# Kernel optimization log

Hardware: AMD Instinct MI355X
Metric: run time of the kernel (lower is better)

Reference implementation:

```python
import jax, jax.numpy as jnp
import numpy as np
import math
from jax import lax

B, L, C_IN = 32, 1024, 21
D_MODEL, N_HEADS, D_FF = 512, 8, 2048
E_LAYERS, FACTOR, MA_K = 3, 1, 25
N_CLASSES = 10
EPS = 1e-5


def setup_inputs() -> dict:
    key = jax.random.key(0)
    ks = jax.random.split(key, 12)
    s = 0.02
    return {
        "x_enc": jax.random.normal(ks[0], (B, L, C_IN), jnp.float32),
        "x_mark_enc": jnp.ones((B, L), jnp.float32),
        "conv_emb_w": jax.random.normal(ks[1], (D_MODEL, C_IN, 3), jnp.float32) * s,
        "Wq": jax.random.normal(ks[2], (E_LAYERS, D_MODEL, D_MODEL), jnp.float32) * s,
        "bq": jnp.zeros((E_LAYERS, D_MODEL), jnp.float32),
        "Wk": jax.random.normal(ks[3], (E_LAYERS, D_MODEL, D_MODEL), jnp.float32) * s,
        "bk": jnp.zeros((E_LAYERS, D_MODEL), jnp.float32),
        "Wv": jax.random.normal(ks[4], (E_LAYERS, D_MODEL, D_MODEL), jnp.float32) * s,
        "bv": jnp.zeros((E_LAYERS, D_MODEL), jnp.float32),
        "Wo": jax.random.normal(ks[5], (E_LAYERS, D_MODEL, D_MODEL), jnp.float32) * s,
        "bo": jnp.zeros((E_LAYERS, D_MODEL), jnp.float32),
        "Wff1": jax.random.normal(ks[6], (E_LAYERS, D_FF, D_MODEL), jnp.float32) * s,
        "Wff2": jax.random.normal(ks[7], (E_LAYERS, D_MODEL, D_FF), jnp.float32) * s,
        "ln_g": jnp.ones((D_MODEL,), jnp.float32),
        "ln_b": jnp.zeros((D_MODEL,), jnp.float32),
        "Wproj": jax.random.normal(ks[8], (N_CLASSES, D_MODEL * L), jnp.float32) * 0.001,
        "bproj": jnp.zeros((N_CLASSES,), jnp.float32),
    }


def token_embed(x, w):
    # x: [B, L, C] -> Conv1d(C->D, k=3, circular padding, no bias) -> [B, L, D]
    xp = jnp.pad(x.transpose(0, 2, 1), ((0, 0), (0, 0), (1, 1)), mode='wrap')  # [B,C,L+2]
    y = lax.conv_general_dilated(xp, w, (1,), 'VALID', dimension_numbers=('NCH', 'OIH', 'NCH'))
    return y.transpose(0, 2, 1)


def moving_avg(x, k):
    # replicate-pad then avg-pool with stride 1 (kernel k odd -> same length)
    pad = (k - 1) // 2
    xp = jnp.concatenate([jnp.repeat(x[:, :1], pad, 1), x, jnp.repeat(x[:, -1:], pad, 1)], axis=1)
    return lax.reduce_window(xp, 0.0, lax.add, (1, k, 1), (1, 1, 1), 'VALID') / k


def series_decomp(x, k):
    m = moving_avg(x, k)
    return x - m, m


def auto_correlation(q, k, v):
    # q,k,v: [B, L, H, E]; FFT-based period correlation + time-delay aggregation (inference variant)
    B_, L_, H, E = q.shape
    qf = jnp.fft.rfft(q.transpose(0, 2, 3, 1), axis=-1)   # [B,H,E,Lf]
    kf = jnp.fft.rfft(k.transpose(0, 2, 3, 1), axis=-1)
    corr = jnp.fft.irfft(qf * jnp.conj(kf), n=L_, axis=-1)  # [B,H,E,L]
    values = v.transpose(0, 2, 3, 1)                        # [B,H,E,L]
    mean_value = corr.mean(axis=(1, 2))                     # [B,L]
    top_k = int(FACTOR * math.log(L_))
    weights, delay = lax.top_k(mean_value, top_k)           # [B,k]
    tmp_corr = jax.nn.softmax(weights, axis=-1)
    tmp_values = jnp.concatenate([values, values], axis=-1)  # [B,H,E,2L]
    init_index = jnp.arange(L_)
    agg = jnp.zeros_like(values)
    for i in range(top_k):  # small fixed loop (top_k = 6)
        idx = init_index[None, :] + delay[:, i:i + 1]        # [B,L]
        idx_b = jnp.broadcast_to(idx[:, None, None, :], (B_, H, E, L_))
        pat = jnp.take_along_axis(tmp_values, idx_b, axis=-1)
        agg = agg + pat * tmp_corr[:, i][:, None, None, None]
    return agg.transpose(0, 3, 1, 2)  # [B,L,H,E]


def encoder_layer(x, Wq, bq, Wk, bk, Wv, bv, Wo, bo, Wf1, Wf2):
    B_, L_, D = x.shape
    E = D // N_HEADS
    q = (x @ Wq.T + bq).reshape(B_, L_, N_HEADS, E)
    k = (x @ Wk.T + bk).reshape(B_, L_, N_HEADS, E)
    v = (x @ Wv.T + bv).reshape(B_, L_, N_HEADS, E)
    a = auto_correlation(q, k, v).reshape(B_, L_, D)
    a = a @ Wo.T + bo
    x = x + a
    x, _ = series_decomp(x, MA_K)
    y = jax.nn.gelu(jnp.einsum('bld,fd->blf', x, Wf1), approximate=False)
    y = jnp.einsum('blf,df->bld', y, Wf2)
    res, _ = series_decomp(x + y, MA_K)
    return res


def my_layernorm(x, g, b):
    mu = x.mean(-1, keepdims=True)
    var = ((x - mu) ** 2).mean(-1, keepdims=True)
    xh = (x - mu) / jnp.sqrt(var + EPS) * g + b
    return xh - xh.mean(axis=1, keepdims=True)  # special LN: remove seq-wise mean


def reference(x_enc, x_mark_enc, conv_emb_w, Wq, bq, Wk, bk, Wv, bv, Wo, bo, Wff1, Wff2, ln_g, ln_b, Wproj, bproj):
    x = token_embed(x_enc, conv_emb_w)  # DataEmbedding_wo_pos with x_mark=None
    for l in range(E_LAYERS):
        x = encoder_layer(x, Wq[l], bq[l], Wk[l], bk[l], Wv[l], bv[l], Wo[l], bo[l], Wff1[l], Wff2[l])
    x = my_layernorm(x, ln_g, ln_b)
    out = jax.nn.gelu(x, approximate=False)
    out = out * x_mark_enc[:, :, None]
    out = out.reshape(out.shape[0], -1)
    return out @ Wproj.T + bproj
```

## Files before the change

### kernel.cpp

```cpp
#include <hip/hip_runtime.h>
#include <cstdint>


using u16 = unsigned short;
typedef _Float16 f16x8 __attribute__((ext_vector_type(8)));
typedef float f32x4 __attribute__((ext_vector_type(4)));

#define BB 32
#define LL 1024
#define DD 512
#define DFF 2048

__device__ __forceinline__ float bf2f(u16 u) {
  union { uint32_t i; float f; } v; v.i = ((uint32_t)u) << 16; return v.f;
}
__device__ __forceinline__ u16 f2bf(float f) {
  union { float f; uint32_t i; } v; v.f = f;
  uint32_t r = (v.i + 0x7FFFu + ((v.i >> 16) & 1u)) >> 16;
  return (u16)r;
}
__device__ __forceinline__ float ldi(const void* p, long i, int isf) {
  return isf ? ((const float*)p)[i] : bf2f(((const u16*)p)[i]);
}
__device__ __forceinline__ float gelu_f(float x) {
  return 0.5f * x * (1.0f + erff(x * 0.70710678118654752440f));
}
__device__ __forceinline__ void gld16(const void* g, void* l) {
  __builtin_amdgcn_global_load_lds(
      (const __attribute__((address_space(1))) void*)g,
      (__attribute__((address_space(3))) void*)l, 16, 0, 0);
}

union H8 { f16x8 v; uint4 u; _Float16 h[8]; };
union H4 { uint2 u; _Float16 h[4]; };

__global__ void detect_k(const uint32_t* __restrict__ mark, int* __restrict__ FLAG) {
  if (threadIdx.x == 0) FLAG[0] = (mark[0] == 0x3F800000u) ? 1 : 0;
}

__global__ __launch_bounds__(256) void wT_k(const void* __restrict__ w,
                                            float* __restrict__ wT,
                                            const int* __restrict__ FLAG) {
  const int isf = *FLAG;
  int idx = blockIdx.x * 256 + threadIdx.x;
  if (idx >= 63 * DD) return;
  int c3t = idx / DD;
  int d = idx - c3t * DD;
  wT[idx] = ldi(w, (long)d * 63 + c3t, isf);
}

__global__ __launch_bounds__(256) void conv_embed_k(
    const void* __restrict__ xe, const float* __restrict__ wT,
    float* __restrict__ X, _Float16* __restrict__ XH, _Float16* __restrict__ XL,
    const int* __restrict__ FLAG) {
  const int isf = *FLAG;
  int b = blockIdx.y;
  int l0 = blockIdx.x * 16;
  __shared__ float xs[18][21];
  int tid = threadIdx.x;
  for (int i = tid; i < 18 * 21; i += 256) {
    int r = i / 21, c = i % 21;
    int row = (l0 - 1 + r + LL) & (LL - 1);
    xs[r][c] = ldi(xe, ((long)b * LL + row) * 21 + c, isf);
  }
  __syncthreads();
  float acc0[16], acc1[16];
#pragma unroll
  for (int ll = 0; ll < 16; ll++) { acc0[ll] = 0.0f; acc1[ll] = 0.0f; }
  for (int c = 0; c < 21; c++) {
    float xreg[18];
#pragma unroll
    for (int r = 0; r < 18; r++) xreg[r] = xs[r][c];
#pragma unroll
    for (int t = 0; t < 3; t++) {
      float w0 = wT[(c * 3 + t) * DD + tid];
      float w1 = wT[(c * 3 + t) * DD + tid + 256];
#pragma unroll
      for (int ll = 0; ll < 16; ll++) {
        acc0[ll] = fmaf(w0, xreg[t + ll], acc0[ll]);
        acc1[ll] = fmaf(w1, xreg[t + ll], acc1[ll]);
      }
    }
  }
#pragma unroll
  for (int ll = 0; ll < 16; ll++) {
    long base = ((long)b * LL + l0 + ll) * DD;
    float v0 = acc0[ll], v1 = acc1[ll];
    X[base + tid] = v0;
    X[base + tid + 256] = v1;
    _Float16 h0 = (_Float16)v0, h1 = (_Float16)v1;
    XH[base + tid] = h0;
    XH[base + tid + 256] = h1;
    XL[base + tid] = (_Float16)((v0 - (float)h0) * 512.0f);
    XL[base + tid + 256] = (_Float16)((v1 - (float)h1) * 512.0f);
  }
}

__global__ __launch_bounds__(256) void tsplit2_k(
    const void* __restrict__ W1, const void* __restrict__ W2, long off,
    _Float16* __restrict__ T1H, _Float16* __restrict__ T1L,
    _Float16* __restrict__ T2H, _Float16* __restrict__ T2L,
    const int* __restrict__ FLAG) {
  const int isf = *FLAG;
  const void* W = blockIdx.z ? W2 : W1;
  _Float16* TH = blockIdx.z ? T2H : T1H;
  _Float16* TL = blockIdx.z ? T2L : T1L;
  __shared__ float t[64][65];
  const int f0 = blockIdx.x * 64, m0 = blockIdx.y * 64;
  const int tid = threadIdx.x;
  const int c = tid & 63, rb = tid >> 6;
#pragma unroll
  for (int r = rb; r < 64; r += 4)
    t[r][c] = ldi(W, off + (long)(f0 + r) * DD + m0 + c, isf);
  __syncthreads();
#pragma unroll
  for (int r = rb; r < 64; r += 4) {
    float v = t[c][r];
    long o = (long)(m0 + r) * DD + f0 + c;
    _Float16 hv = (_Float16)v;
    TH[o] = hv;
    TL[o] = (_Float16)((v - (float)hv) * 512.0f);
  }
}

__global__ __launch_bounds__(256) void split_k(const float* __restrict__ src,
                                               _Float16* __restrict__ dh,
                                               _Float16* __restrict__ dl, int n) {
  long i = ((long)blockIdx.x * 256 + threadIdx.x) * 8;
  if (i >= n) return;
  float4 a = *(const float4*)(src + i);
  float4 b = *(const float4*)(src + i + 4);
  float x[8] = {a.x, a.y, a.z, a.w, b.x, b.y, b.z, b.w};
  H8 h, l;
#pragma unroll
  for (int j = 0; j < 8; j++) {
    _Float16 hv = (_Float16)x[j];
    h.h[j] = hv;
    l.h[j] = (_Float16)((x[j] - (float)hv) * 512.0f);
  }
  *(uint4*)(dh + i) = h.u;
  *(uint4*)(dl + i) = l.u;
}

__global__ __launch_bounds__(256) void wcvt6_k(
    const void* __restrict__ Wv, const void* __restrict__ Wo,
    const void* __restrict__ W1, const void* __restrict__ W2,
    long oW, long oF,
    _Float16* __restrict__ Wvh, _Float16* __restrict__ Woh,
    _Float16* __restrict__ W1h, _Float16* __restrict__ W2h,
    const int* __restrict__ FLAG) {
  const int isf = *FLAG;
  long e = ((long)blockIdx.x * 256 + threadIdx.x) * 8;
  const void* src; long soff; _Float16* dst;
  if (e < 262144) { src = Wv; soff = oW + e; dst = Wvh + e; }
  else if (e < 524288) { src = Wo; soff = oW + (e - 262144); dst = Woh + (e - 262144); }
  else if (e < 1572864) { src = W1; soff = oF + (e - 524288); dst = W1h + (e - 524288); }
  else { src = W2; soff = oF + (e - 1572864); dst = W2h + (e - 1572864); }
  H8 r;
  if (isf) {
    const float* s = (const float*)src + soff;
    float4 a = *(const float4*)s;
    float4 b = *(const float4*)(s + 4);
    r.h[0] = (_Float16)a.x; r.h[1] = (_Float16)a.y;
    r.h[2] = (_Float16)a.z; r.h[3] = (_Float16)a.w;
    r.h[4] = (_Float16)b.x; r.h[5] = (_Float16)b.y;
    r.h[6] = (_Float16)b.z; r.h[7] = (_Float16)b.w;
  } else {
    const u16* s = (const u16*)src + soff;
    uint4 u = *(const uint4*)s;
    r.h[0] = (_Float16)bf2f((u16)(u.x & 0xffff));
    r.h[1] = (_Float16)bf2f((u16)(u.x >> 16));
    r.h[2] = (_Float16)bf2f((u16)(u.y & 0xffff));
    r.h[3] = (_Float16)bf2f((u16)(u.y >> 16));
    r.h[4] = (_Float16)bf2f((u16)(u.z & 0xffff));
    r.h[5] = (_Float16)bf2f((u16)(u.z >> 16));
    r.h[6] = (_Float16)bf2f((u16)(u.w & 0xffff));
    r.h[7] = (_Float16)bf2f((u16)(u.w >> 16));
  }
  *(uint4*)(dst) = r.u;
}

__global__ __launch_bounds__(256) void gemm_z(
    const _Float16* __restrict__ Ah, const _Float16* __restrict__ Al,
    const _Float16* __restrict__ Bh, const _Float16* __restrict__ Bl,
    _Float16* __restrict__ Zh, _Float16* __restrict__ Zl,
    int M, int N, int K) {
  __shared__ __align__(16) _Float16 AsH[128 * 32];
  __shared__ __align__(16) _Float16 AsL[128 * 32];
  __shared__ __align__(16) _Float16 BsH[128 * 32];
  __shared__ __align__(16) _Float16 BsL[128 * 32];
  const int n0 = blockIdx.x * 128, m0 = blockIdx.y * 128;
  const int tid = threadIdx.x;
  const int lane = tid & 63, wvi = tid >> 6;
  const int wm = (wvi >> 1) * 64, wn = (wvi & 1) * 64;
  const int l15 = lane & 15, quad = lane >> 4;
  const int ib = wvi * 128 + lane;
  const int r0 = ib >> 2, r1 = r0 + 16;
  const int c0 = ((ib & 3) ^ ((r0 >> 1) & 3)) * 8;
  const int c1 = ((ib & 3) ^ ((r1 >> 1) & 3)) * 8;
  const int lb0 = wvi * 1024, lb1 = wvi * 1024 + 512;
  const long ga0 = (long)(m0 + r0) * K + c0;
  const long ga1 = (long)(m0 + r1) * K + c1;
  const long gb0 = (long)(n0 + r0) * K + c0;
  const long gb1 = (long)(n0 + r1) * K + c1;
  f32x4 aM[4][4], aC[4][4];
#pragma unroll
  for (int i = 0; i < 4; i++)
#pragma unroll
    for (int j = 0; j < 4; j++) {
      aM[i][j] = (f32x4){0.f, 0.f, 0.f, 0.f};
      aC[i][j] = (f32x4){0.f, 0.f, 0.f, 0.f};
    }
  for (int k0 = 0; k0 < K; k0 += 32) {
    __syncthreads();
    gld16(Ah + ga0 + k0, AsH + lb0);
    gld16(Ah + ga1 + k0, AsH + lb1);
    gld16(Al + ga0 + k0, AsL + lb0);
    gld16(Al + ga1 + k0, AsL + lb1);
    gld16(Bh + gb0 + k0, BsH + lb0);
    gld16(Bh + gb1 + k0, BsH + lb1);
    gld16(Bl + gb0 + k0, BsL + lb0);
    gld16(Bl + gb1 + k0, BsL + lb1);
    __syncthreads();
    f16x8 fah[4], fal[4], fbh[4], fbl[4];
#pragma unroll
    for (int mi = 0; mi < 4; mi++) {
      int r = wm + mi * 16 + l15;
      int o = r * 32 + ((quad ^ ((r >> 1) & 3)) * 8);
      fah[mi] = *(const f16x8*)&AsH[o];
      fal[mi] = *(const f16x8*)&AsL[o];
    }
#pragma unroll
    for (int ni = 0; ni < 4; ni++) {
      int r = wn + ni * 16 + l15;
      int o = r * 32 + ((quad ^ ((r >> 1) & 3)) * 8);
      fbh[ni] = *(const f16x8*)&BsH[o];
      fbl[ni] = *(const f16x8*)&BsL[o];
    }
#pragma unroll
    for (int mi = 0; mi < 4; mi++)
#pragma unroll
      for (int ni = 0; ni < 4; ni++) {
        aM[mi][ni] = __builtin_amdgcn_mfma_f32_16x16x32_f16(
            fah[mi], fbh[ni], aM[mi][ni], 0, 0, 0);
        aC[mi][ni] = __builtin_amdgcn_mfma_f32_16x16x32_f16(
            fah[mi], fbl[ni], aC[mi][ni], 0, 0, 0);
        aC[mi][ni] = __builtin_amdgcn_mfma_f32_16x16x32_f16(
            fal[mi], fbh[ni], aC[mi][ni], 0, 0, 0);
      }
  }
#pragma unroll
  for (int mi = 0; mi < 4; mi++) {
    int rowg = m0 + wm + mi * 16 + quad * 4;
#pragma unroll
    for (int ni = 0; ni < 4; ni++) {
      int colg = n0 + wn + ni * 16 + l15;
#pragma unroll
      for (int rr = 0; rr < 4; rr++) {
        long off = (long)(rowg + rr) * N + colg;
        float z = aM[mi][ni][rr] + aC[mi][ni][rr] * (1.0f / 512.0f);
        _Float16 zh = (_Float16)z;
        Zh[off] = zh;
        Zl[off] = (_Float16)((z - (float)zh) * 512.0f);
      }
    }
  }
}

__global__ __launch_bounds__(256) void qkmv_hl(
    const _Float16* __restrict__ Zh, const _Float16* __restrict__ Zl,
    const _Float16* __restrict__ Xh, const _Float16* __restrict__ Xl,
    float* __restrict__ MV) {
  __shared__ __align__(16) _Float16 AsH[128 * 32];
  __shared__ __align__(16) _Float16 AsL[128 * 32];
  __shared__ __align__(16) _Float16 BsH[128 * 32];
  __shared__ __align__(16) _Float16 BsL[128 * 32];
  __shared__ float diag[255];
  const int bz = blockIdx.z;
  const long bb = (long)bz * LL * DD;
  const int n0 = blockIdx.x * 128, m0 = blockIdx.y * 128;
  const int tid = threadIdx.x;
  const int lane = tid & 63, wvi = tid >> 6;
  const int wm = (wvi >> 1) * 64, wn = (wvi & 1) * 64;
  const int l15 = lane & 15, quad = lane >> 4;
  const int ib = wvi * 128 + lane;
  const int r0 = ib >> 2, r1 = r0 + 16;
  const int c0 = ((ib & 3) ^ ((r0 >> 1) & 3)) * 8;
  const int c1 = ((ib & 3) ^ ((r1 >> 1) & 3)) * 8;
  const int lb0 = wvi * 1024, lb1 = wvi * 1024 + 512;
  const long ga0 = bb + (long)(m0 + r0) * DD + c0;
  const long ga1 = bb + (long)(m0 + r1) * DD + c1;
  const long gb0 = bb + (long)(n0 + r0) * DD + c0;
  const long gb1 = bb + (long)(n0 + r1) * DD + c1;
  if (tid < 255) diag[tid] = 0.0f;
  f32x4 aM[4][4], aC[4][4];
#pragma unroll
  for (int i = 0; i < 4; i++)
#pragma unroll
    for (int j = 0; j < 4; j++) {
      aM[i][j] = (f32x4){0.f, 0.f, 0.f, 0.f};
      aC[i][j] = (f32x4){0.f, 0.f, 0.f, 0.f};
    }
  for (int k0 = 0; k0 < DD; k0 += 32) {
    __syncthreads();
    gld16(Zh + ga0 + k0, AsH + lb0);
    gld16(Zh + ga1 + k0, AsH + lb1);
    gld16(Zl + ga0 + k0, AsL + lb0);
    gld16(Zl + ga1 + k0, AsL + lb1);
    gld16(Xh + gb0 + k0, BsH + lb0);
    gld16(Xh + gb1 + k0, BsH + lb1);
    gld16(Xl + gb0 + k0, BsL + lb0);
    gld16(Xl + gb1 + k0, BsL + lb1);
    __syncthreads();
    f16x8 fah[4], fal[4], fbh[4], fbl[4];
#pragma unroll
    for (int mi = 0; mi < 4; mi++) {
      int r = wm + mi * 16 + l15;
      int o = r * 32 + ((quad ^ ((r >> 1) & 3)) * 8);
      fah[mi] = *(const f16x8*)&AsH[o];
      fal[mi] = *(const f16x8*)&AsL[o];
    }
#pragma unroll
    for (int ni = 0; ni < 4; ni++) {
      int r = wn + ni * 16 + l15;
      int o = r * 32 + ((quad ^ ((r >> 1) & 3)) * 8);
      fbh[ni] = *(const f16x8*)&BsH[o];
      fbl[ni] = *(const f16x8*)&BsL[o];
    }
#pragma unroll
    for (int mi = 0; mi < 4; mi++)
#pragma unroll
      for (int ni = 0; ni < 4; ni++) {
        aM[mi][ni] = __builtin_amdgcn_mfma_f32_16x16x32_f16(
            fah[mi], fbh[ni], aM[mi][ni], 0, 0, 0);
        aC[mi][ni] = __builtin_amdgcn_mfma_f32_16x16x32_f16(
            fah[mi], fbl[ni], aC[mi][ni], 0, 0, 0);
        aC[mi][ni] = __builtin_amdgcn_mfma_f32_16x16x32_f16(
            fal[mi], fbh[ni], aC[mi][ni], 0, 0, 0);
      }
  }
#pragma unroll
  for (int g = -3; g <= 3; g++) {
#pragma unroll
    for (int rr = 0; rr < 4; rr++) {
      float s = 0.0f;
#pragma unroll
      for (int mi = 0; mi < 4; mi++) {
        int ni = mi - g;
        if (ni >= 0 && ni < 4)
          s += aM[mi][ni][rr] + aC[mi][ni][rr] * (1.0f / 512.0f);
      }
      int d = 127 + (wm - wn) + g * 16 + quad * 4 + rr - l15;
      atomicAdd(&diag[d], s);
    }
  }
  __syncthreads();
  if (tid < 255) {
    int tau = (m0 - n0 + tid - 127 + LL) & (LL - 1);
    atomicAdd(&MV[(long)bz * LL + tau], diag[tid] * (1.0f / 512.0f));
  }
}

template <int FLAGS>
__global__ __launch_bounds__(256) void gemm_h(
    const void* __restrict__ Av, const _Float16* __restrict__ W,
    const void* __restrict__ biasBase, long bOff,
    const float* __restrict__ R, void* __restrict__ Cout,
    int M, int N, int K, const int* __restrict__ FLAG) {
  constexpr bool HAS_BIAS = (FLAGS & 1) != 0;
  constexpr bool DO_GELU = (FLAGS & 2) != 0;
  constexpr bool DO_RES = (FLAGS & 4) != 0;
  constexpr bool OUT_H = (FLAGS & 8) != 0;
  constexpr bool A_F32 = (FLAGS & 16) != 0;
  __shared__ __align__(16) _Float16 As[128 * 64];
  __shared__ __align__(16) _Float16 Bs[128 * 64];
  const int n0 = blockIdx.x * 128, m0 = blockIdx.y * 128;
  const int tid = threadIdx.x;
  const int lane = tid & 63, wvi = tid >> 6;
  const int wm = (wvi >> 1) * 64, wn = (wvi & 1) * 64;
  const int l15 = lane & 15, quad = lane >> 4;
  const _Float16* gA[4];
  const float* gAf[4];
  const _Float16* gB[4];
  int ldsOff[4];
#pragma unroll
  for (int j = 0; j < 4; j++) {
    int ib = wvi * 256 + j * 64 + lane;
    int row = ib >> 3, p = ib & 7;
    int gc = ((p & 4) | ((p & 3) ^ ((row >> 1) & 3))) * 8;
    if constexpr (A_F32) gAf[j] = (const float*)Av + (long)(m0 + row) * K + gc;
    else gA[j] = (const _Float16*)Av + (long)(m0 + row) * K + gc;
    gB[j] = W + (long)(n0 + row) * K + gc;
    ldsOff[j] = wvi * 2048 + j * 512;
  }
  f32x4 acc[4][4];
#pragma unroll
  for (int i = 0; i < 4; i++)
#pragma unroll
    for (int j = 0; j < 4; j++) acc[i][j] = (f32x4){0.f, 0.f, 0.f, 0.f};
  for (int k0 = 0; k0 < K; k0 += 64) {
    __syncthreads();
#pragma unroll
    for (int j = 0; j < 4; j++) gld16(gB[j] + k0, Bs + ldsOff[j]);
    if constexpr (A_F32) {
#pragma unroll
      for (int j = 0; j < 4; j++) {
        const float* s = gAf[j] + k0;
        float4 p0 = *(const float4*)s;
        float4 p1 = *(const float4*)(s + 4);
        H8 h;
        h.h[0] = (_Float16)p0.x; h.h[1] = (_Float16)p0.y;
        h.h[2] = (_Float16)p0.z; h.h[3] = (_Float16)p0.w;
        h.h[4] = (_Float16)p1.x; h.h[5] = (_Float16)p1.y;
        h.h[6] = (_Float16)p1.z; h.h[7] = (_Float16)p1.w;
        *(uint4*)&As[ldsOff[j] + lane * 8] = h.u;
      }
    } else {
#pragma unroll
      for (int j = 0; j < 4; j++) gld16(gA[j] + k0, As + ldsOff[j]);
    }
    __syncthreads();
#pragma unroll
    for (int ks = 0; ks < 2; ks++) {
      f16x8 af[4], bfr[4];
#pragma unroll
      for (int mi = 0; mi < 4; mi++) {
        int r = wm + mi * 16 + l15;
        af[mi] = *(const f16x8*)&As[r * 64 + (ks * 4 + (quad ^ ((r >> 1) & 3))) * 8];
      }
#pragma unroll
      for (int ni = 0; ni < 4; ni++) {
        int r = wn + ni * 16 + l15;
        bfr[ni] = *(const f16x8*)&Bs[r * 64 + (ks * 4 + (quad ^ ((r >> 1) & 3))) * 8];
      }
#pragma unroll
      for (int mi = 0; mi < 4; mi++)
#pragma unroll
        for (int ni = 0; ni < 4; ni++)
          acc[mi][ni] = __builtin_amdgcn_mfma_f32_16x16x32_f16(
              af[mi], bfr[ni], acc[mi][ni], 0, 0, 0);
    }
  }
  float bcol[4];
  if constexpr (HAS_BIAS) {
    const int isf = *FLAG;
#pragma unroll
    for (int ni = 0; ni < 4; ni++)
      bcol[ni] = ldi(biasBase, bOff + n0 + wn + ni * 16 + l15, isf);
  }
#pragma unroll
  for (int mi = 0; mi < 4; mi++) {
    int rowg = m0 + wm + mi * 16 + quad * 4;
#pragma unroll
    for (int ni = 0; ni < 4; ni++) {
      int colg = n0 + wn + ni * 16 + l15;
#pragma unroll
      for (int rr = 0; rr < 4; rr++) {
        long off = (long)(rowg + rr) * N + colg;
        float v = acc[mi][ni][rr];
        if constexpr (HAS_BIAS) v += bcol[ni];
        if constexpr (DO_RES) v += R[off];
        if constexpr (DO_GELU) v = gelu_f(v);
        if constexpr (OUT_H) ((_Float16*)Cout)[off] = (_Float16)v;
        else ((float*)Cout)[off] = v;
      }
    }
  }
}

__global__ __launch_bounds__(256) void topk_k(const float* __restrict__ MV,
                                              float* __restrict__ WGT,
                                              int* __restrict__ DLY) {
  int b = blockIdx.x;
  __shared__ float vals[LL];
  __shared__ float rv[256];
  __shared__ int ri[256];
  __shared__ float selv[6];
  int tid = threadIdx.x;
  for (int i = tid; i < LL; i += 256) vals[i] = MV[(long)b * LL + i];
  __syncthreads();
  for (int it = 0; it < 6; it++) {
    float bv = -1e30f;
    int bi = LL - 1;
    for (int i = tid; i < LL; i += 256) {
      float v = vals[i];
      if (v > bv || (v == bv && i < bi)) { bv = v; bi = i; }
    }
    rv[tid] = bv; ri[tid] = bi;
    __syncthreads();
    for (int st = 128; st > 0; st >>= 1) {
      if (tid < st) {
        float ov = rv[tid + st]; int oi = ri[tid + st];
        if (ov > rv[tid] || (ov == rv[tid] && oi < ri[tid])) {
          rv[tid] = ov; ri[tid] = oi;
        }
      }
      __syncthreads();
    }
    if (tid == 0) {
      selv[it] = rv[0];
      DLY[b * 6 + it] = ri[0];
      vals[ri[0]] = -1e30f;
    }
    __syncthreads();
  }
  if (tid == 0) {
    float mx = selv[0];
    float e[6], s = 0.0f;
    for (int i = 0; i < 6; i++) { e[i] = expf(selv[i] - mx); s += e[i]; }
    for (int i = 0; i < 6; i++) WGT[b * 6 + i] = e[i] / s;
  }
}

__global__ __launch_bounds__(128) void agg_k(const _Float16* __restrict__ V,
                                             const float* __restrict__ WGT,
                                             const int* __restrict__ DLY,
                                             _Float16* __restrict__ O) {
  int l = blockIdx.x, b = blockIdx.y;
  int tid = threadIdx.x;
  float w[6]; int dl[6];
#pragma unroll
  for (int i = 0; i < 6; i++) { w[i] = WGT[b * 6 + i]; dl[i] = DLY[b * 6 + i]; }
  long base = (long)b * LL * DD;
  int d = tid * 4;
  float a0 = 0, a1 = 0, a2 = 0, a3 = 0;
#pragma unroll
  for (int i = 0; i < 6; i++) {
    int row = (l + dl[i]) & (LL - 1);
    H4 t; t.u = *(const uint2*)&V[base + (long)row * DD + d];
    a0 += w[i] * (float)t.h[0];
    a1 += w[i] * (float)t.h[1];
    a2 += w[i] * (float)t.h[2];
    a3 += w[i] * (float)t.h[3];
  }
  H4 r;
  r.h[0] = (_Float16)a0; r.h[1] = (_Float16)a1;
  r.h[2] = (_Float16)a2; r.h[3] = (_Float16)a3;
  *(uint2*)&O[base + (long)l * DD + d] = r.u;
}

__global__ __launch_bounds__(256) void decomp_k(const float* __restrict__ Xin,
                                                float* __restrict__ Out) {
  int d = blockIdx.x * 256 + threadIdx.x;
  int l0 = blockIdx.y * 64;
  int b = blockIdx.z;
  const float* xb = Xin + (long)b * LL * DD + d;
  float* ob = Out + (long)b * LL * DD + d;
  float wsum = 0.0f;
  for (int j = l0 - 12; j <= l0 + 12; j++) {
    int jj = min(max(j, 0), LL - 1);
    wsum += xb[(long)jj * DD];
  }
  for (int l = l0; l < l0 + 64; l++) {
    float xv = xb[(long)l * DD];
    ob[(long)l * DD] = xv - wsum * (1.0f / 25.0f);
    int ja = min(l + 13, LL - 1);
    int jr = max(l - 12, 0);
    wsum += xb[(long)ja * DD] - xb[(long)jr * DD];
  }
}

__global__ __launch_bounds__(256) void ln_k(const float* __restrict__ X,
                                            const void* __restrict__ g,
                                            const void* __restrict__ be,
                                            float* __restrict__ XHo,
                                            const int* __restrict__ FLAG) {
  const int isf = *FLAG;
  int l = blockIdx.x, b = blockIdx.y;
  const float* xr = X + ((long)b * LL + l) * DD;
  int tid = threadIdx.x;
  float x0 = xr[tid], x1 = xr[tid + 256];
  __shared__ float rs[256], rq[256];
  rs[tid] = x0 + x1;
  rq[tid] = x0 * x0 + x1 * x1;
  __syncthreads();
  for (int st = 128; st > 0; st >>= 1) {
    if (tid < st) { rs[tid] += rs[tid + st]; rq[tid] += rq[tid + st]; }
    __syncthreads();
  }
  float mu = rs[0] * (1.0f / 512.0f);
  float var = rq[0] * (1.0f / 512.0f) - mu * mu;
  float rstd = rsqrtf(var + 1e-5f);
  float* o = XHo + ((long)b * LL + l) * DD;
  o[tid] = (x0 - mu) * rstd * ldi(g, tid, isf) + ldi(be, tid, isf);
  o[tid + 256] = (x1 - mu) * rstd * ldi(g, tid + 256, isf) + ldi(be, tid + 256, isf);
}

__global__ __launch_bounds__(256) void colmean_k(const float* __restrict__ XHo,
                                                 float* __restrict__ CMp) {
  int d = blockIdx.x * 256 + threadIdx.x;
  int part = blockIdx.y;
  int b = blockIdx.z;
  const float* p = XHo + (long)b * LL * DD + (long)part * 128 * DD + d;
  float s = 0.0f;
  for (int l = 0; l < 128; l++) s += p[(long)l * DD];
  CMp[((long)part * BB + b) * DD + d] = s;
}

__global__ __launch_bounds__(256) void geluout_k(const float* __restrict__ XHo,
                                                 const float* __restrict__ CMp,
                                                 const void* __restrict__ mark,
                                                 float* __restrict__ OUT,
                                                 const int* __restrict__ FLAG) {
  const int isf = *FLAG;
  int l = blockIdx.x, b = blockIdx.y;
  int tid = threadIdx.x;
  float mk = ldi(mark, (long)b * LL + l, isf);
  long off = ((long)b * LL + l) * DD;
#pragma unroll
  for (int h = 0; h < 2; h++) {
    int d = tid + h * 256;
    float cs = 0.0f;
#pragma unroll
    for (int p = 0; p < 8; p++) cs += CMp[((long)p * BB + b) * DD + d];
    float v = XHo[off + d] - cs * (1.0f / 1024.0f);
    OUT[off + d] = gelu_f(v) * mk;
  }
}

__global__ __launch_bounds__(256) void proj1_k(const float* __restrict__ OUT,
                                               const void* __restrict__ Wp,
                                               float* __restrict__ PB2,
                                               const int* __restrict__ FLAG) {
  const int isf = *FLAG;
  const int blk = blockIdx.x;
  const int tid = threadIdx.x;
  const int wave = tid >> 6, lane = tid & 63;
  const int grp = lane >> 4, ln = lane & 15;
  const long e = (long)blk * 1024 + tid * 4;
  float w[10][4];
  if (isf) {
    const float* wp = (const float*)Wp;
#pragma unroll
    for (int n = 0; n < 10; n++) {
      float4 t = *(const float4*)&wp[(long)n * 524288 + e];
      w[n][0] = t.x; w[n][1] = t.y; w[n][2] = t.z; w[n][3] = t.w;
    }
  } else {
    const u16* wp = (const u16*)Wp;
#pragma unroll
    for (int n = 0; n < 10; n++) {
      uint2 u = *(const uint2*)&wp[(long)n * 524288 + e];
      w[n][0] = bf2f((u16)(u.x & 0xffff));
      w[n][1] = bf2f((u16)(u.x >> 16));
      w[n][2] = bf2f((u16)(u.y & 0xffff));
      w[n][3] = bf2f((u16)(u.y >> 16));
    }
  }
  __shared__ float sm[4][4][BB][16];
  float4 xn = *(const float4*)&OUT[e];
  for (int b = 0; b < BB; b++) {
    float4 x = xn;
    if (b < BB - 1) xn = *(const float4*)&OUT[(long)(b + 1) * 524288 + e];
    float acc[10];
#pragma unroll
    for (int n = 0; n < 10; n++)
      acc[n] = x.x * w[n][0] + x.y * w[n][1] + x.z * w[n][2] + x.w * w[n][3];
#pragma unroll
    for (int s = 1; s <= 8; s <<= 1)
#pragma unroll
      for (int n = 0; n < 10; n++) acc[n] += __shfl_xor(acc[n], s, 64);
    float v = 0.0f;
#pragma unroll
    for (int n = 0; n < 10; n++) v = (ln == n) ? acc[n] : v;
    if (ln < 10) sm[wave][grp][b][ln] = v;
  }
  __syncthreads();
  for (int o = tid; o < BB * 10; o += 256) {
    int b = o / 10, n = o - b * 10;
    float s = 0.0f;
#pragma unroll
    for (int w4 = 0; w4 < 4; w4++)
#pragma unroll
      for (int g = 0; g < 4; g++) s += sm[w4][g][b][n];
    PB2[(long)o * 512 + blk] = s;
  }
}

__global__ __launch_bounds__(64) void proj2_k(const float* __restrict__ PB2,
                                              const void* __restrict__ bp,
                                              void* __restrict__ out,
                                              const int* __restrict__ FLAG) {
  const int isf = *FLAG;
  int n = blockIdx.x, b = blockIdx.y;
  int o = b * 10 + n;
  int tid = threadIdx.x;
  float s = 0.0f;
  for (int j = tid; j < 512; j += 64) s += PB2[(long)o * 512 + j];
#pragma unroll
  for (int st = 32; st > 0; st >>= 1) s += __shfl_xor(s, st, 64);
  if (tid == 0) {
    s += ldi(bp, n, isf);
    if (isf) ((float*)out)[o] = s;
    else ((u16*)out)[o] = f2bf(s);
  }
}

extern "C" void kernel_launch(void* const* d_in, const int* in_sizes, int n_in,
                              void* d_out, int out_size, void* d_ws, size_t ws_size,
                              hipStream_t stream) {
  const void* xe = d_in[0];
  const void* mark = d_in[1];
  const void* cw = d_in[2];
  const void* Wq = d_in[3];
  const void* Wk = d_in[5];
  const void* Wv = d_in[7];
  const void* bv = d_in[8];
  const void* Wo = d_in[9];
  const void* bo = d_in[10];
  const void* Wff1 = d_in[11];
  const void* Wff2 = d_in[12];
  const void* lng = d_in[13];
  const void* lnb = d_in[14];
  const void* Wp = d_in[15];
  const void* bp = d_in[16];

  char* ws = (char*)d_ws;
  float* X      = (float*)(ws + 0L);
  _Float16* XH  = (_Float16*)(ws + 67108864L);
  _Float16* XL  = (_Float16*)(ws + 100663296L);
  _Float16* AGh = (_Float16*)(ws + 100663296L);
  _Float16* ZH  = (_Float16*)(ws + 134217728L);
  _Float16* ZL  = (_Float16*)(ws + 138412032L);
  _Float16* Ph  = (_Float16*)(ws + 134217728L);
  float* CMp    = (float*)(ws + 134217728L);
  float* wT     = (float*)(ws + 142606336L);
  _Float16* KTH = (_Float16*)(ws + 142606336L);
  _Float16* KTL = (_Float16*)(ws + 143130624L);
  _Float16* QTH = (_Float16*)(ws + 143654912L);
  _Float16* QTL = (_Float16*)(ws + 144179200L);
  _Float16* GH  = (_Float16*)(ws + 144703488L);
  _Float16* GL  = (_Float16*)(ws + 145227776L);
  _Float16* Wvh = (_Float16*)(ws + 142606336L);
  _Float16* Woh = (_Float16*)(ws + 143130624L);
  _Float16* W1h = (_Float16*)(ws + 143654912L);
  _Float16* W2h = (_Float16*)(ws + 145752064L);
  float* MV  = (float*)(ws + 147849216L);
  float* WGT = (float*)(ws + 147980288L);
  int*   DLY = (int*)(ws + 147981312L);
  int*  FLAG = (int*)(ws + 148068352L);
  float* S2  = (float*)(ws + 67108864L);
  float* PB2 = (float*)(ws + 67108864L);
  _Float16* Hb = (_Float16*)X;

  const long AD = (long)LL * DD;
  const int M = BB * LL;

  detect_k<<<1, 64, 0, stream>>>((const uint32_t*)mark, FLAG);
  wT_k<<<126, 256, 0, stream>>>(cw, wT, FLAG);
  conv_embed_k<<<dim3(64, 32), 256, 0, stream>>>(xe, wT, X, XH, XL, FLAG);

  for (int l = 0; l < 3; l++) {
    const long oW = (long)l * DD * DD;
    const long oB = (long)l * DD;
    const long oF = (long)l * DFF * DD;

    tsplit2_k<<<dim3(8, 8, 2), 256, 0, stream>>>(Wk, Wq, oW,
                                                 KTH, KTL, QTH, QTL, FLAG);
    gemm_z<<<dim3(4, 4), 256, 0, stream>>>(KTH, KTL, QTH, QTL,
                                           GH, GL, 512, 512, 512);
    hipMemsetAsync(MV, 0, (long)BB * LL * sizeof(float), stream);
    for (int cb = 0; cb < 8; cb++) {
      const long co = (long)cb * 4 * AD;
      gemm_z<<<dim3(4, 32), 256, 0, stream>>>(
          XH + co, XL + co, GH, GL, ZH, ZL, 4096, DD, DD);
      qkmv_hl<<<dim3(8, 8, 4), 256, 0, stream>>>(
          ZH, ZL, XH + co, XL + co, MV + (long)cb * 4 * LL);
    }
    topk_k<<<32, 256, 0, stream>>>(MV, WGT, DLY);

    wcvt6_k<<<1280, 256, 0, stream>>>(Wv, Wo, Wff1, Wff2, oW, oF,
                                      Wvh, Woh, W1h, W2h, FLAG);

    for (int cb = 0; cb < 4; cb++) {
      const _Float16* xh = XH + (long)cb * 8 * AD;
      gemm_h<1 | 8><<<dim3(4, 64), 256, 0, stream>>>(
          xh, Wvh, bv, oB, nullptr, Ph, 8192, DD, DD, FLAG);
      agg_k<<<dim3(1024, 8), 128, 0, stream>>>(
          Ph, WGT + cb * 48, DLY + cb * 48, AGh + (long)cb * 8 * AD);
    }

    gemm_h<1 | 4><<<dim3(4, 256), 256, 0, stream>>>(
        AGh, Woh, bo, oB, X, X, M, DD, DD, FLAG);

    decomp_k<<<dim3(2, 16, 32), 256, 0, stream>>>(X, S2);

    for (int cb = 0; cb < 4; cb++) {
      float* xd = S2 + (long)cb * 8 * AD;
      gemm_h<2 | 8 | 16><<<dim3(16, 64), 256, 0, stream>>>(
          xd, W1h, nullptr, 0, nullptr, Hb, 8192, DFF, DD, FLAG);
      gemm_h<4><<<dim3(4, 64), 256, 0, stream>>>(
          Hb, W2h, nullptr, 0, xd, xd, 8192, DD, DFF, FLAG);
    }

    decomp_k<<<dim3(2, 16, 32), 256, 0, stream>>>(S2, X);
    if (l < 2) split_k<<<8192, 256, 0, stream>>>(X, XH, XL, 16777216);
  }

  ln_k<<<dim3(1024, 32), 256, 0, stream>>>(X, lng, lnb, S2, FLAG);
  colmean_k<<<dim3(2, 8, 32), 256, 0, stream>>>(S2, CMp);
  geluout_k<<<dim3(1024, 32), 256, 0, stream>>>(S2, CMp, mark, X, FLAG);
  proj1_k<<<512, 256, 0, stream>>>(X, Wp, PB2, FLAG);
  proj2_k<<<dim3(10, 32), 64, 0, stream>>>(PB2, bp, d_out, FLAG);
}
```

Measured before the change: 3.582 ms.

## Add grid swizzle to GEMMs and async-load fp32 A tiles for FF1 GEMM

Adds an XCD-aware block-index swizzle (groups of 8) to the GEMM kernels so that neighbouring tiles land on the same chiplet and share L2. Replaces the FF1 GEMM's synchronous fp32 A loads, converted to fp16 before the LDS store, with a dedicated kernel. That kernel streams fp32 A tiles straight into swizzled LDS via global_load_lds and converts to fp16 when reading fragments, using a K-step of 32. This removes register staging and conversion from the load path, at the cost of twice the LDS bytes for A and more sync iterations.

```diff
diff --git a/kernel.cpp b/kernel.cpp
--- a/kernel.cpp
+++ b/kernel.cpp
@@ -29,6 +29,15 @@
   __builtin_amdgcn_global_load_lds(
       (const __attribute__((address_space(1))) void*)g,
       (__attribute__((address_space(3))) void*)l, 16, 0, 0);
+}
+__device__ __forceinline__ void swz8(int& bx, int& by) {
+  int gx = gridDim.x;
+  int nwg = gx * gridDim.y;
+  int bid = by * gx + bx;
+  int q = nwg >> 3;
+  int s = (bid & 7) * q + (bid >> 3);
+  bx = s % gx;
+  by = s / gx;
 }
 
 union H8 { f16x8 v; uint4 u; _Float16 h[8]; };
@@ -189,7 +198,9 @@
   __shared__ __align__(16) _Float16 AsL[128 * 32];
   __shared__ __align__(16) _Float16 BsH[128 * 32];
   __shared__ __align__(16) _Float16 BsL[128 * 32];
-  const int n0 = blockIdx.x * 128, m0 = blockIdx.y * 128;
+  int bx = blockIdx.x, by = blockIdx.y;
+  swz8(bx, by);
+  const int n0 = bx * 128, m0 = by * 128;
   const int tid = threadIdx.x;
   const int lane = tid & 63, wvi = tid >> 6;
   const int wm = (wvi >> 1) * 64, wn = (wvi & 1) * 64;
@@ -363,7 +374,7 @@
 
 template <int FLAGS>
 __global__ __launch_bounds__(256) void gemm_h(
-    const void* __restrict__ Av, const _Float16* __restrict__ W,
+    const _Float16* __restrict__ A, const _Float16* __restrict__ W,
     const void* __restrict__ biasBase, long bOff,
     const float* __restrict__ R, void* __restrict__ Cout,
     int M, int N, int K, const int* __restrict__ FLAG) {
@@ -371,16 +382,16 @@
   constexpr bool DO_GELU = (FLAGS & 2) != 0;
   constexpr bool DO_RES = (FLAGS & 4) != 0;
   constexpr bool OUT_H = (FLAGS & 8) != 0;
-  constexpr bool A_F32 = (FLAGS & 16) != 0;
   __shared__ __align__(16) _Float16 As[128 * 64];
   __shared__ __align__(16) _Float16 Bs[128 * 64];
-  const int n0 = blockIdx.x * 128, m0 = blockIdx.y * 128;
+  int bx = blockIdx.x, by = blockIdx.y;
+  swz8(bx, by);
+  const int n0 = bx * 128, m0 = by * 128;
   const int tid = threadIdx.x;
   const int lane = tid & 63, wvi = tid >> 6;
   const int wm = (wvi >> 1) * 64, wn = (wvi & 1) * 64;
   const int l15 = lane & 15, quad = lane >> 4;
   const _Float16* gA[4];
-  const float* gAf[4];
   const _Float16* gB[4];
   int ldsOff[4];
 #pragma unroll
@@ -388,8 +399,7 @@
     int ib = wvi * 256 + j * 64 + lane;
     int row = ib >> 3, p = ib & 7;
     int gc = ((p & 4) | ((p & 3) ^ ((row >> 1) & 3))) * 8;
-    if constexpr (A_F32) gAf[j] = (const float*)Av + (long)(m0 + row) * K + gc;
-    else gA[j] = (const _Float16*)Av + (long)(m0 + row) * K + gc;
+    gA[j] = A + (long)(m0 + row) * K + gc;
     gB[j] = W + (long)(n0 + row) * K + gc;
     ldsOff[j] = wvi * 2048 + j * 512;
   }
@@ -401,24 +411,9 @@
   for (int k0 = 0; k0 < K; k0 += 64) {
     __syncthreads();
 #pragma unroll
+    for (int j = 0; j < 4; j++) gld16(gA[j] + k0, As + ldsOff[j]);
+#pragma unroll
     for (int j = 0; j < 4; j++) gld16(gB[j] + k0, Bs + ldsOff[j]);
-    if constexpr (A_F32) {
-#pragma unroll
-      for (int j = 0; j < 4; j++) {
-        const float* s = gAf[j] + k0;
-        float4 p0 = *(const float4*)s;
-        float4 p1 = *(const float4*)(s + 4);
-        H8 h;
-        h.h[0] = (_Float16)p0.x; h.h[1] = (_Float16)p0.y;
-        h.h[2] = (_Float16)p0.z; h.h[3] = (_Float16)p0.w;
-        h.h[4] = (_Float16)p1.x; h.h[5] = (_Float16)p1.y;
-        h.h[6] = (_Float16)p1.z; h.h[7] = (_Float16)p1.w;
-        *(uint4*)&As[ldsOff[j] + lane * 8] = h.u;
-      }
-    } else {
-#pragma unroll
-      for (int j = 0; j < 4; j++) gld16(gA[j] + k0, As + ldsOff[j]);
-    }
     __syncthreads();
 #pragma unroll
     for (int ks = 0; ks < 2; ks++) {
@@ -463,6 +458,89 @@
         if constexpr (DO_GELU) v = gelu_f(v);
         if constexpr (OUT_H) ((_Float16*)Cout)[off] = (_Float16)v;
         else ((float*)Cout)[off] = v;
+      }
+    }
+  }
+}
+
+__global__ __launch_bounds__(256) void gemm_hf(
+    const float* __restrict__ A, const _Float16* __restrict__ W,
+    _Float16* __restrict__ Cout, int M, int N, int K) {
+  __shared__ __align__(16) float As32[128 * 32];
+  __shared__ __align__(16) _Float16 Bs[128 * 32];
+  int bx = blockIdx.x, by = blockIdx.y;
+  swz8(bx, by);
+  const int n0 = bx * 128, m0 = by * 128;
+  const int tid = threadIdx.x;
+  const int lane = tid & 63, wvi = tid >> 6;
+  const int wm = (wvi >> 1) * 64, wn = (wvi & 1) * 64;
+  const int l15 = lane & 15, quad = lane >> 4;
+  const float* gAf[4];
+#pragma unroll
+  for (int j = 0; j < 4; j++) {
+    int ib = j * 256 + tid;
+    int row = ib >> 3, p = ib & 7;
+    int gs = p ^ (row & 7);
+    gAf[j] = A + (long)(m0 + row) * K + gs * 4;
+  }
+  const int ibb = wvi * 128 + lane;
+  const int r0 = ibb >> 2, r1 = r0 + 16;
+  const int c0 = ((ibb & 3) ^ ((r0 >> 1) & 3)) * 8;
+  const int c1 = ((ibb & 3) ^ ((r1 >> 1) & 3)) * 8;
+  const int lb0 = wvi * 1024, lb1 = wvi * 1024 + 512;
+  const long gb0 = (long)(n0 + r0) * K + c0;
+  const long gb1 = (long)(n0 + r1) * K + c1;
+  f32x4 acc[4][4];
+#pragma unroll
+  for (int i = 0; i < 4; i++)
+#pragma unroll
+    for (int j = 0; j < 4; j++) acc[i][j] = (f32x4){0.f, 0.f, 0.f, 0.f};
+  for (int k0 = 0; k0 < K; k0 += 32) {
+    __syncthreads();
+#pragma unroll
+    for (int j = 0; j < 4; j++)
+      gld16(gAf[j] + k0, As32 + j * 1024 + wvi * 256);
+    gld16(W + gb0 + k0, Bs + lb0);
+    gld16(W + gb1 + k0, Bs + lb1);
+    __syncthreads();
+    f16x8 af[4], bf[4];
+#pragma unroll
+    for (int mi = 0; mi < 4; mi++) {
+      int r = wm + mi * 16 + l15;
+      int p0 = (2 * quad) ^ (r & 7);
+      int p1 = (2 * quad + 1) ^ (r & 7);
+      f32x4 v0 = *(const f32x4*)&As32[r * 32 + p0 * 4];
+      f32x4 v1 = *(const f32x4*)&As32[r * 32 + p1 * 4];
+      H8 h;
+      h.h[0] = (_Float16)v0[0]; h.h[1] = (_Float16)v0[1];
+      h.h[2] = (_Float16)v0[2]; h.h[3] = (_Float16)v0[3];
+      h.h[4] = (_Float16)v1[0]; h.h[5] = (_Float16)v1[1];
+      h.h[6] = (_Float16)v1[2]; h.h[7] = (_Float16)v1[3];
+      af[mi] = h.v;
+    }
+#pragma unroll
+    for (int ni = 0; ni < 4; ni++) {
+      int r = wn + ni * 16 + l15;
+      int o = r * 32 + ((quad ^ ((r >> 1) & 3)) * 8);
+      bf[ni] = *(const f16x8*)&Bs[o];
+    }
+#pragma unroll
+    for (int mi = 0; mi < 4; mi++)
+#pragma unroll
+      for (int ni = 0; ni < 4; ni++)
+        acc[mi][ni] = __builtin_amdgcn_mfma_f32_16x16x32_f16(
+            af[mi], bf[ni], acc[mi][ni], 0, 0, 0);
+  }
+#pragma unroll
+  for (int mi = 0; mi < 4; mi++) {
+    int rowg = m0 + wm + mi * 16 + quad * 4;
+#pragma unroll
+    for (int ni = 0; ni < 4; ni++) {
+      int colg = n0 + wn + ni * 16 + l15;
+#pragma unroll
+      for (int rr = 0; rr < 4; rr++) {
+        float v = gelu_f(acc[mi][ni][rr]);
+        Cout[(long)(rowg + rr) * N + colg] = (_Float16)v;
       }
     }
   }
@@ -787,8 +865,8 @@
 
     for (int cb = 0; cb < 4; cb++) {
       float* xd = S2 + (long)cb * 8 * AD;
-      gemm_h<2 | 8 | 16><<<dim3(16, 64), 256, 0, stream>>>(
-          xd, W1h, nullptr, 0, nullptr, Hb, 8192, DFF, DD, FLAG);
+      gemm_hf<<<dim3(16, 64), 256, 0, stream>>>(
+          xd, W1h, Hb, 8192, DFF, DD);
       gemm_h<4><<<dim3(4, 64), 256, 0, stream>>>(
           Hb, W2h, nullptr, 0, xd, xd, 8192, DD, DFF, FLAG);
     }
```

Result: no change. 3.594 ms (+0.3%).
